# Performance work log

Hardware: AMD Instinct MI355X
Metric: run time of the kernel (lower is better)

The kernel has to match this reference:

```python
import jax, jax.numpy as jnp
import numpy as np

B, T, E, H = 128, 256, 512, 8
D = E // H  # head_dim = 64
F = 4 * E   # ffn hidden = 2048
EPS = 1e-5


def layer_norm(x, g, b):
    mu = jnp.mean(x, axis=-1, keepdims=True)
    var = jnp.mean(jnp.square(x - mu), axis=-1, keepdims=True)
    return (x - mu) * jax.lax.rsqrt(var + EPS) * g + b


def setup_inputs() -> dict:
    key = jax.random.key(0)
    ks = jax.random.split(key, 12)
    s_e = 1.0 / np.sqrt(E)
    s_f = 1.0 / np.sqrt(F)
    return {
        "x": jax.random.normal(ks[0], (B, T, E), dtype=jnp.float32),
        "Wq": jax.random.uniform(ks[1], (H, E, D), jnp.float32, -s_e, s_e),
        "Wk": jax.random.uniform(ks[2], (H, E, D), jnp.float32, -s_e, s_e),
        "Wv": jax.random.uniform(ks[3], (H, E, D), jnp.float32, -s_e, s_e),
        "Wo": jax.random.uniform(ks[4], (E, E), jnp.float32, -s_e, s_e),
        "bo": jax.random.uniform(ks[5], (E,), jnp.float32, -s_e, s_e),
        "ln1_g": jnp.ones((E,), jnp.float32),
        "ln1_b": jnp.zeros((E,), jnp.float32),
        "ln2_g": jnp.ones((E,), jnp.float32),
        "ln2_b": jnp.zeros((E,), jnp.float32),
        "W1": jax.random.uniform(ks[6], (E, F), jnp.float32, -s_e, s_e),
        "b1": jax.random.uniform(ks[7], (F,), jnp.float32, -s_e, s_e),
        "W2": jax.random.uniform(ks[8], (F, E), jnp.float32, -s_f, s_f),
        "b2": jax.random.uniform(ks[9], (E,), jnp.float32, -s_f, s_f),
    }


def reference(x, Wq, Wk, Wv, Wo, bo, ln1_g, ln1_b, ln2_g, ln2_b, W1, b1, W2, b2):
    # --- multi-head causal self-attention on ln1(x) (dropout = identity, eval mode) ---
    h = layer_norm(x, ln1_g, ln1_b)                       # [B,T,E]
    q = jnp.einsum('bte,hed->bhtd', h, Wq)
    k = jnp.einsum('bte,hed->bhtd', h, Wk)
    v = jnp.einsum('bte,hed->bhtd', h, Wv)
    scores = jnp.einsum('bhtd,bhsd->bhts', q, k) * (D ** -0.5)  # [B,H,T,T]
    causal = jnp.tril(jnp.ones((T, T), dtype=bool))
    scores = jnp.where(causal, scores, -jnp.inf)
    attn = jax.nn.softmax(scores, axis=-1)
    ctx = jnp.einsum('bhts,bhsd->bhtd', attn, v)          # [B,H,T,D]
    ctx = jnp.transpose(ctx, (0, 2, 1, 3)).reshape(B, T, E)  # concat heads
    x = ctx @ Wo + bo + x
    # --- FFN on ln2(x) ---
    h2 = layer_norm(x, ln2_g, ln2_b)
    ff = jax.nn.relu(h2 @ W1 + b1) @ W2 + b2
    return x + ff
```

## Files before the change

kernel.cpp:

```cpp
#include <hip/hip_runtime.h>


typedef unsigned short u16;
typedef short short8 __attribute__((ext_vector_type(8)));
typedef float f32x4 __attribute__((ext_vector_type(4)));

#define BB 128
#define TT 256
#define EE 512
#define HH 8
#define DD 64
#define FF 2048
#define BT (BB * TT)

__device__ __forceinline__ u16 f2b(float f) {
  union { float f; unsigned int u; } v; v.f = f;
  unsigned int u = v.u + 0x7fffu + ((v.u >> 16) & 1u);
  return (u16)(u >> 16);
}

__device__ __forceinline__ f32x4 mfma16(short8 a, short8 b, f32x4 c) {
  return __builtin_amdgcn_mfma_f32_16x16x32_bf16(a, b, c, 0, 0, 0);
}

__device__ __forceinline__ void g2l16(const u16* g, u16* l) {
  __builtin_amdgcn_global_load_lds(
      (const __attribute__((address_space(1))) unsigned int*)g,
      (__attribute__((address_space(3))) unsigned int*)l, 16, 0, 0);
}


__global__ __launch_bounds__(256) void tconv(const float* __restrict__ src, int srs,
                                             u16* __restrict__ dst, int drs) {
  __shared__ u16 tile[64][67];
  const int r0 = blockIdx.x * 64, c0 = blockIdx.y * 64;
  const int tlo = threadIdx.x & 63, thi = threadIdx.x >> 6;
#pragma unroll
  for (int i = 0; i < 16; i++) {
    const int r = i * 4 + thi;
    tile[r][tlo] = f2b(src[(size_t)(r0 + r) * srs + c0 + tlo]);
  }
  __syncthreads();
#pragma unroll
  for (int i = 0; i < 16; i++) {
    const int c = i * 4 + thi;
    dst[(size_t)(c0 + c) * drs + r0 + tlo] = tile[tlo][c];
  }
}

__global__ __launch_bounds__(256) void tconv_qkv(const float* __restrict__ W,
                                                 u16* __restrict__ dst0, int nbase) {
  __shared__ u16 tile[64][67];
  const int h = blockIdx.z;
  const float* src = W + (size_t)h * EE * DD;
  u16* dst = dst0 + (size_t)(nbase + h * 64) * EE;
  const int r0 = blockIdx.x * 64;
  const int tlo = threadIdx.x & 63, thi = threadIdx.x >> 6;
#pragma unroll
  for (int i = 0; i < 16; i++) {
    const int r = i * 4 + thi;
    tile[r][tlo] = f2b(src[(size_t)(r0 + r) * DD + tlo]);
  }
  __syncthreads();
#pragma unroll
  for (int i = 0; i < 16; i++) {
    const int d = i * 4 + thi;
    dst[(size_t)d * EE + r0 + tlo] = tile[tlo][d];
  }
}


__global__ __launch_bounds__(256) void ln_fwd(const float* __restrict__ xin,
                                              const float* __restrict__ g,
                                              const float* __restrict__ bb,
                                              u16* __restrict__ out) {
  const int wid = threadIdx.x >> 6, lane = threadIdx.x & 63;
  const size_t row = (size_t)blockIdx.x * 4 + wid;
  const float* xr = xin + row * EE + lane * 8;
  float v[8];
  *(float4*)(v)     = *(const float4*)(xr);
  *(float4*)(v + 4) = *(const float4*)(xr + 4);
  float s = 0.f;
#pragma unroll
  for (int j = 0; j < 8; j++) s += v[j];
#pragma unroll
  for (int d = 1; d < 64; d <<= 1) s += __shfl_xor(s, d);
  const float mu = s * (1.f / 512.f);
  float q = 0.f;
#pragma unroll
  for (int j = 0; j < 8; j++) { float dd = v[j] - mu; q += dd * dd; }
#pragma unroll
  for (int d = 1; d < 64; d <<= 1) q += __shfl_xor(q, d);
  const float rstd = rsqrtf(q * (1.f / 512.f) + 1e-5f);
  float gv[8], bv[8];
  *(float4*)(gv)     = *(const float4*)(g + lane * 8);
  *(float4*)(gv + 4) = *(const float4*)(g + lane * 8 + 4);
  *(float4*)(bv)     = *(const float4*)(bb + lane * 8);
  *(float4*)(bv + 4) = *(const float4*)(bb + lane * 8 + 4);
  short8 o;
#pragma unroll
  for (int j = 0; j < 8; j++) o[j] = (short)f2b((v[j] - mu) * rstd * gv[j] + bv[j]);
  *(short8*)(out + row * EE + lane * 8) = o;
}


template <bool BIAS, bool RELU, bool RES, bool OUTBF>
__global__ __launch_bounds__(256) void gemm_bt(const u16* __restrict__ A,
                                               const u16* __restrict__ Bt,
                                               const float* __restrict__ bias,
                                               const float* __restrict__ res,
                                               void* __restrict__ out,
                                               int M, int N, int K) {
  __shared__ u16 As[128 * 32];
  __shared__ u16 Bs[128 * 32];
  const int tid = threadIdx.x;
  const int wid = tid >> 6, lane = tid & 63;
  const int llo = lane & 15, lhi = lane >> 4;
  const int wr = (wid >> 1) * 64, wc = (wid & 1) * 64;

  const int gx = gridDim.x;
  const int nwg = gx * gridDim.y;
  int id = blockIdx.y * gx + blockIdx.x;
  id = (id & 7) * (nwg >> 3) + (id >> 3);
  const size_t row0 = (size_t)(id / gx) * 128;
  const size_t col0 = (size_t)(id % gx) * 128;

  f32x4 acc[4][4];
#pragma unroll
  for (int m = 0; m < 4; m++)
#pragma unroll
    for (int n = 0; n < 4; n++) acc[m][n] = (f32x4){0.f, 0.f, 0.f, 0.f};

  for (int k0 = 0; k0 < K; k0 += 32) {
    __syncthreads();
#pragma unroll
    for (int i = 0; i < 2; i++) {
      const int cb = i * 256 + wid * 64;
      const int c = cb + lane;
      g2l16(A + (row0 + (c >> 2)) * K + k0 + (c & 3) * 8, As + cb * 8);
      g2l16(Bt + (col0 + (c >> 2)) * K + k0 + (c & 3) * 8, Bs + cb * 8);
    }
    __syncthreads();
    short8 af[4], bf[4];
#pragma unroll
    for (int m = 0; m < 4; m++) af[m] = *(const short8*)(As + (wr + m * 16 + llo) * 32 + lhi * 8);
#pragma unroll
    for (int n = 0; n < 4; n++) bf[n] = *(const short8*)(Bs + (wc + n * 16 + llo) * 32 + lhi * 8);
#pragma unroll
    for (int m = 0; m < 4; m++)
#pragma unroll
      for (int n = 0; n < 4; n++) acc[m][n] = mfma16(af[m], bf[n], acc[m][n]);
  }

#pragma unroll
  for (int m = 0; m < 4; m++)
#pragma unroll
    for (int r = 0; r < 4; r++) {
      const size_t row = row0 + wr + m * 16 + lhi * 4 + r;
#pragma unroll
      for (int n = 0; n < 4; n++) {
        const size_t col = col0 + wc + n * 16 + llo;
        float v = acc[m][n][r];
        if (BIAS) v += bias[col];
        if (RELU) v = fmaxf(v, 0.f);
        if (RES) v += res[row * (size_t)N + col];
        if (OUTBF) ((u16*)out)[row * (size_t)N + col] = f2b(v);
        else       ((float*)out)[row * (size_t)N + col] = v;
      }
    }
}


__global__ __launch_bounds__(256) void attn_fwd(const u16* __restrict__ qkv,
                                                u16* __restrict__ ctx) {
  const int bh = blockIdx.x;
  const int b = bh >> 3, h = bh & 7;
  const int wid = threadIdx.x >> 6;
  const int lane = threadIdx.x & 63;
  const int llo = lane & 15, lhi = lane >> 4;
  const int t0 = wid * 64;

  __shared__ u16 Vt[64][264];
  __shared__ u16 Pl[4][64][32];

  const u16* qp = qkv + (size_t)b * TT * 1536 + h * 64;
  const u16* kp = qp + 512;
  const u16* vp = qp + 1024;

  {
    const int j = lane & 7;
#pragma unroll
    for (int g8 = 0; g8 < 8; g8++) {
      const int s = wid * 64 + g8 * 8 + (lane >> 3);
      const short8 v = *(const short8*)(vp + (size_t)s * 1536 + j * 8);
#pragma unroll
      for (int jj = 0; jj < 8; jj++) Vt[j * 8 + jj][s] = (u16)v[jj];
    }
  }

  short8 qf[4][2];
#pragma unroll
  for (int m = 0; m < 4; m++)
#pragma unroll
    for (int k2 = 0; k2 < 2; k2++) {
      const int t = t0 + m * 16 + llo;
      qf[m][k2] = *(const short8*)(qp + (size_t)t * 1536 + k2 * 32 + lhi * 8);
    }

  f32x4 O[4][4];
  float mrow[4][4], lrow[4][4];
#pragma unroll
  for (int m = 0; m < 4; m++) {
#pragma unroll
    for (int n = 0; n < 4; n++) O[m][n] = (f32x4){0.f, 0.f, 0.f, 0.f};
#pragma unroll
    for (int r = 0; r < 4; r++) { mrow[m][r] = -1e30f; lrow[m][r] = 0.f; }
  }

  __syncthreads();

  const int nst = (t0 + 64) >> 5;
  for (int st = 0; st < nst; st++) {
    const int s0 = st * 32;
    f32x4 S[4][2];
#pragma unroll
    for (int m = 0; m < 4; m++) {
      S[m][0] = (f32x4){0.f, 0.f, 0.f, 0.f};
      S[m][1] = (f32x4){0.f, 0.f, 0.f, 0.f};
    }
#pragma unroll
    for (int k2 = 0; k2 < 2; k2++) {
      const short8 b0 = *(const short8*)(kp + (size_t)(s0 + llo) * 1536 + k2 * 32 + lhi * 8);
      const short8 b1 = *(const short8*)(kp + (size_t)(s0 + 16 + llo) * 1536 + k2 * 32 + lhi * 8);
#pragma unroll
      for (int m = 0; m < 4; m++) {
        S[m][0] = mfma16(qf[m][k2], b0, S[m][0]);
        S[m][1] = mfma16(qf[m][k2], b1, S[m][1]);
      }
    }
#pragma unroll
    for (int m = 0; m < 4; m++) {
      float sf[4];
#pragma unroll
      for (int r = 0; r < 4; r++) {
        const int t = t0 + m * 16 + lhi * 4 + r;
        float v0 = S[m][0][r] * 0.125f;
        float v1 = S[m][1][r] * 0.125f;
        if (s0 + llo > t)      v0 = -1e30f;
        if (s0 + 16 + llo > t) v1 = -1e30f;
        float mx = fmaxf(v0, v1);
#pragma unroll
        for (int d = 1; d < 16; d <<= 1) mx = fmaxf(mx, __shfl_xor(mx, d));
        const float mnew = fmaxf(mrow[m][r], mx);
        const float sc = __expf(mrow[m][r] - mnew);
        mrow[m][r] = mnew;
        const float p0 = __expf(v0 - mnew);
        const float p1 = __expf(v1 - mnew);
        float rs = p0 + p1;
#pragma unroll
        for (int d = 1; d < 16; d <<= 1) rs += __shfl_xor(rs, d);
        lrow[m][r] = lrow[m][r] * sc + rs;
        sf[r] = sc;
        const int pr = m * 16 + lhi * 4 + r;
        Pl[wid][pr][llo]      = f2b(p0);
        Pl[wid][pr][llo + 16] = f2b(p1);
      }
#pragma unroll
      for (int n = 0; n < 4; n++)
#pragma unroll
        for (int r = 0; r < 4; r++) O[m][n][r] *= sf[r];
    }
    short8 pf[4];
#pragma unroll
    for (int m = 0; m < 4; m++)
      pf[m] = *(const short8*)(&Pl[wid][m * 16 + llo][lhi * 8]);
#pragma unroll
    for (int n = 0; n < 4; n++) {
      const short8 vf = *(const short8*)(&Vt[n * 16 + llo][s0 + lhi * 8]);
#pragma unroll
      for (int m = 0; m < 4; m++) O[m][n] = mfma16(pf[m], vf, O[m][n]);
    }
  }

#pragma unroll
  for (int m = 0; m < 4; m++)
#pragma unroll
    for (int r = 0; r < 4; r++) {
      const int t = t0 + m * 16 + lhi * 4 + r;
      const float inv = 1.f / lrow[m][r];
      u16* orow = ctx + ((size_t)b * TT + t) * EE + h * 64;
#pragma unroll
      for (int n = 0; n < 4; n++)
        orow[n * 16 + llo] = f2b(O[m][n][r] * inv);
    }
}


extern "C" void kernel_launch(void* const* d_in, const int* in_sizes, int n_in,
                              void* d_out, int out_size, void* d_ws, size_t ws_size,
                              hipStream_t stream) {
  const float* x   = (const float*)d_in[0];
  const float* Wq  = (const float*)d_in[1];
  const float* Wk  = (const float*)d_in[2];
  const float* Wv  = (const float*)d_in[3];
  const float* Wo  = (const float*)d_in[4];
  const float* bo  = (const float*)d_in[5];
  const float* g1  = (const float*)d_in[6];
  const float* be1 = (const float*)d_in[7];
  const float* g2  = (const float*)d_in[8];
  const float* be2 = (const float*)d_in[9];
  const float* W1  = (const float*)d_in[10];
  const float* b1  = (const float*)d_in[11];
  const float* W2  = (const float*)d_in[12];
  const float* b2  = (const float*)d_in[13];
  float* out = (float*)d_out;

  char* w = (char*)d_ws;
  u16* WqkvT = (u16*)w;                 w += (size_t)1536 * 512 * 2;
  u16* WoT   = (u16*)w;                 w += (size_t)512 * 512 * 2;
  u16* W1T   = (u16*)w;                 w += (size_t)2048 * 512 * 2;
  u16* W2T   = (u16*)w;                 w += (size_t)512 * 2048 * 2;
  u16* hbuf  = (u16*)w;                 w += (size_t)BT * EE * 2;
  u16* ctxb  = (u16*)w;                 w += (size_t)BT * EE * 2;
  u16* big   = (u16*)w;
  u16* qkvb = big;
  u16* ff1  = big;

  tconv_qkv<<<dim3(8, 1, 8), 256, 0, stream>>>(Wq, WqkvT, 0);
  tconv_qkv<<<dim3(8, 1, 8), 256, 0, stream>>>(Wk, WqkvT, 512);
  tconv_qkv<<<dim3(8, 1, 8), 256, 0, stream>>>(Wv, WqkvT, 1024);
  tconv<<<dim3(8, 8),  256, 0, stream>>>(Wo, 512,  WoT, 512);
  tconv<<<dim3(8, 32), 256, 0, stream>>>(W1, 2048, W1T, 512);
  tconv<<<dim3(32, 8), 256, 0, stream>>>(W2, 512,  W2T, 2048);

  ln_fwd<<<BT / 4, 256, 0, stream>>>(x, g1, be1, hbuf);

  gemm_bt<false, false, false, true><<<dim3(1536 / 128, BT / 128), 256, 0, stream>>>(
      hbuf, WqkvT, nullptr, nullptr, qkvb, BT, 1536, 512);

  attn_fwd<<<BB * HH, 256, 0, stream>>>(qkvb, ctxb);

  gemm_bt<true, false, true, false><<<dim3(512 / 128, BT / 128), 256, 0, stream>>>(
      ctxb, WoT, bo, x, out, BT, 512, 512);

  ln_fwd<<<BT / 4, 256, 0, stream>>>(out, g2, be2, hbuf);

  gemm_bt<true, true, false, true><<<dim3(2048 / 128, BT / 128), 256, 0, stream>>>(
      hbuf, W1T, b1, nullptr, ff1, BT, 2048, 512);

  gemm_bt<true, false, true, false><<<dim3(512 / 128, BT / 128), 256, 0, stream>>>(
      ff1, W2T, b2, out, out, BT, 512, 2048);
}
```

Baseline: 648.8 us.

## Replace GEMM with triple-buffered 128x256 tile kernel using swizzled LDS

The GEMM kernel is rewritten to use 128x256 output tiles with 8 waves, K-step 64, and a three-stage LDS ring buffer. Global-to-LDS loads for tile t+2 are interleaved with the MFMA work on tile t using explicit vmcnt waits and s_setprio. An XOR swizzle is applied to LDS addresses to avoid bank conflicts. The goal is to hide memory latency and cut barrier overhead. The cost is larger LDS use (144 KB per block) and more fragile hand-tuned synchronisation.

```diff
diff --git a/kernel.cpp b/kernel.cpp
--- a/kernel.cpp
+++ b/kernel.cpp
@@ -105,25 +105,42 @@
 
 
 template <bool BIAS, bool RELU, bool RES, bool OUTBF>
-__global__ __launch_bounds__(256) void gemm_bt(const u16* __restrict__ A,
-                                               const u16* __restrict__ Bt,
-                                               const float* __restrict__ bias,
-                                               const float* __restrict__ res,
-                                               void* __restrict__ out,
-                                               int M, int N, int K) {
-  __shared__ u16 As[128 * 32];
-  __shared__ u16 Bs[128 * 32];
+__global__ __launch_bounds__(512, 2) void gemm3(const u16* __restrict__ A,
+                                                const u16* __restrict__ Bt,
+                                                const float* __restrict__ bias,
+                                                const float* __restrict__ res,
+                                                void* __restrict__ out,
+                                                int M, int N, int K) {
+  __shared__ __align__(16) u16 As[3 * 128 * 64];
+  __shared__ __align__(16) u16 Bs[3 * 256 * 64];
   const int tid = threadIdx.x;
   const int wid = tid >> 6, lane = tid & 63;
   const int llo = lane & 15, lhi = lane >> 4;
-  const int wr = (wid >> 1) * 64, wc = (wid & 1) * 64;
-
-  const int gx = gridDim.x;
-  const int nwg = gx * gridDim.y;
-  int id = blockIdx.y * gx + blockIdx.x;
+  const int wrow = (wid >> 2) * 64;
+  const int wcol = (wid & 3) * 64;
+
+  const int gx = N >> 8;
+  const int nwg = gx * (M >> 7);
+  int id = blockIdx.x;
   id = (id & 7) * (nwg >> 3) + (id >> 3);
   const size_t row0 = (size_t)(id / gx) * 128;
-  const size_t col0 = (size_t)(id % gx) * 128;
+  const size_t col0 = (size_t)(id % gx) * 256;
+  const int nt = K >> 6;
+
+  auto stageA = [&](int tt, int c) {
+    const int o = c * 8192 + tid * 16;
+    const int row = o >> 7;
+    const int colb = (o & 127) ^ ((row & 7) << 4);
+    g2l16(A + (row0 + row) * (size_t)K + (size_t)(tt << 6) + (colb >> 1),
+          As + (tt % 3) * 8192 + c * 4096 + (wid << 9));
+  };
+  auto stageB = [&](int tt, int c) {
+    const int o = c * 8192 + tid * 16;
+    const int row = o >> 7;
+    const int colb = (o & 127) ^ ((row & 7) << 4);
+    g2l16(Bt + (col0 + row) * (size_t)K + (size_t)(tt << 6) + (colb >> 1),
+          Bs + (tt % 3) * 16384 + c * 4096 + (wid << 9));
+  };
 
   f32x4 acc[4][4];
 #pragma unroll
@@ -131,35 +148,71 @@
 #pragma unroll
     for (int n = 0; n < 4; n++) acc[m][n] = (f32x4){0.f, 0.f, 0.f, 0.f};
 
-  for (int k0 = 0; k0 < K; k0 += 32) {
-    __syncthreads();
-#pragma unroll
-    for (int i = 0; i < 2; i++) {
-      const int cb = i * 256 + wid * 64;
-      const int c = cb + lane;
-      g2l16(A + (row0 + (c >> 2)) * K + k0 + (c & 3) * 8, As + cb * 8);
-      g2l16(Bt + (col0 + (c >> 2)) * K + k0 + (c & 3) * 8, Bs + cb * 8);
-    }
-    __syncthreads();
-    short8 af[4], bf[4];
-#pragma unroll
-    for (int m = 0; m < 4; m++) af[m] = *(const short8*)(As + (wr + m * 16 + llo) * 32 + lhi * 8);
-#pragma unroll
-    for (int n = 0; n < 4; n++) bf[n] = *(const short8*)(Bs + (wc + n * 16 + llo) * 32 + lhi * 8);
+#pragma unroll
+  for (int c = 0; c < 2; c++) stageA(0, c);
+#pragma unroll
+  for (int c = 0; c < 4; c++) stageB(0, c);
+#pragma unroll
+  for (int c = 0; c < 2; c++) stageA(1, c);
+#pragma unroll
+  for (int c = 0; c < 4; c++) stageB(1, c);
+
+  for (int t = 0; t < nt; ++t) {
+    if (t + 1 < nt) asm volatile("s_waitcnt vmcnt(6)" ::: "memory");
+    else            asm volatile("s_waitcnt vmcnt(0)" ::: "memory");
+    __builtin_amdgcn_s_barrier();
+    asm volatile("" ::: "memory");
+    const char* Ab = (const char*)As + (t % 3) * 16384;
+    const char* Bb = (const char*)Bs + (t % 3) * 32768;
+    const bool pf = (t + 2 < nt);
+
+    if (pf) { stageA(t + 2, 0); stageA(t + 2, 1); stageB(t + 2, 0); }
+    short8 a0[4], b0[4];
+#pragma unroll
+    for (int m = 0; m < 4; m++) {
+      const int row = wrow + m * 16 + llo;
+      a0[m] = *(const short8*)(Ab + row * 128 + ((lhi * 16) ^ ((row & 7) << 4)));
+    }
+#pragma unroll
+    for (int n = 0; n < 4; n++) {
+      const int row = wcol + n * 16 + llo;
+      b0[n] = *(const short8*)(Bb + row * 128 + ((lhi * 16) ^ ((row & 7) << 4)));
+    }
+    __builtin_amdgcn_s_setprio(1);
 #pragma unroll
     for (int m = 0; m < 4; m++)
 #pragma unroll
-      for (int n = 0; n < 4; n++) acc[m][n] = mfma16(af[m], bf[n], acc[m][n]);
+      for (int n = 0; n < 4; n++) acc[m][n] = mfma16(a0[m], b0[n], acc[m][n]);
+    __builtin_amdgcn_s_setprio(0);
+
+    if (pf) { stageB(t + 2, 1); stageB(t + 2, 2); stageB(t + 2, 3); }
+    short8 a1[4], b1[4];
+#pragma unroll
+    for (int m = 0; m < 4; m++) {
+      const int row = wrow + m * 16 + llo;
+      a1[m] = *(const short8*)(Ab + row * 128 + ((64 + lhi * 16) ^ ((row & 7) << 4)));
+    }
+#pragma unroll
+    for (int n = 0; n < 4; n++) {
+      const int row = wcol + n * 16 + llo;
+      b1[n] = *(const short8*)(Bb + row * 128 + ((64 + lhi * 16) ^ ((row & 7) << 4)));
+    }
+    __builtin_amdgcn_s_setprio(1);
+#pragma unroll
+    for (int m = 0; m < 4; m++)
+#pragma unroll
+      for (int n = 0; n < 4; n++) acc[m][n] = mfma16(a1[m], b1[n], acc[m][n]);
+    __builtin_amdgcn_s_setprio(0);
   }
 
 #pragma unroll
   for (int m = 0; m < 4; m++)
 #pragma unroll
     for (int r = 0; r < 4; r++) {
-      const size_t row = row0 + wr + m * 16 + lhi * 4 + r;
+      const size_t row = row0 + wrow + m * 16 + lhi * 4 + r;
 #pragma unroll
       for (int n = 0; n < 4; n++) {
-        const size_t col = col0 + wc + n * 16 + llo;
+        const size_t col = col0 + wcol + n * 16 + llo;
         float v = acc[m][n][r];
         if (BIAS) v += bias[col];
         if (RELU) v = fmaxf(v, 0.f);
@@ -335,19 +388,19 @@
 
   ln_fwd<<<BT / 4, 256, 0, stream>>>(x, g1, be1, hbuf);
 
-  gemm_bt<false, false, false, true><<<dim3(1536 / 128, BT / 128), 256, 0, stream>>>(
+  gemm3<false, false, false, true><<<1536, 512, 0, stream>>>(
       hbuf, WqkvT, nullptr, nullptr, qkvb, BT, 1536, 512);
 
   attn_fwd<<<BB * HH, 256, 0, stream>>>(qkvb, ctxb);
 
-  gemm_bt<true, false, true, false><<<dim3(512 / 128, BT / 128), 256, 0, stream>>>(
+  gemm3<true, false, true, false><<<512, 512, 0, stream>>>(
       ctxb, WoT, bo, x, out, BT, 512, 512);
 
   ln_fwd<<<BT / 4, 256, 0, stream>>>(out, g2, be2, hbuf);
 
-  gemm_bt<true, true, false, true><<<dim3(2048 / 128, BT / 128), 256, 0, stream>>>(
+  gemm3<true, true, false, true><<<2048, 512, 0, stream>>>(
       hbuf, W1T, b1, nullptr, ff1, BT, 2048, 512);
 
-  gemm_bt<true, false, true, false><<<dim3(512 / 128, BT / 128), 256, 0, stream>>>(
+  gemm3<true, false, true, false><<<512, 512, 0, stream>>>(
       ff1, W2T, b2, out, out, BT, 512, 2048);
 }
```

Result: no change. 650.5 us (+0.2%).
